# Kernel optimization log

Measured on AMD Instinct MI355X. Metric: run time of the kernel, lower is better.

## Reference

```python
import jax, jax.numpy as jnp
import numpy as np

TEMPERATURE = 8.0  # sqrt(d_k), d_k = 64

def setup_inputs() -> dict:
    key = jax.random.key(0)
    kq, kk, kv, km = jax.random.split(key, 4)
    B, H, S, D = 4, 16, 1024, 64
    q = jax.random.normal(kq, (B, H, S, D), dtype=jnp.float32)
    k = jax.random.normal(kk, (B, H, S, D), dtype=jnp.float32)
    v = jax.random.normal(kv, (B, H, S, D), dtype=jnp.float32)
    mask = jax.random.randint(km, (B, 1, S, S), 0, 2, dtype=jnp.int32)
    return {"q": q, "k": k, "v": v, "mask": mask}

def reference(q, k, v, mask):
    # scores: [B,H,S,S]
    attn = jnp.einsum("bhqd,bhkd->bhqk", q, k) / TEMPERATURE
    attn = jnp.where(mask == 0, jnp.float32(-1e9), attn)
    attn = jax.nn.softmax(attn, axis=-1)
    output = jnp.einsum("bhqk,bhkd->bhqd", attn, v)
    return (output, attn)
```

## Files before the change

### kernel.cpp

```cpp
#include <hip/hip_runtime.h>
#include <hip/hip_bf16.h>

#define S_LEN 1024
#define DH 64
#define QB 64
#define KT 64
#define NKT 16
#define LDP 72

typedef __attribute__((ext_vector_type(8))) short bf16x8;
typedef __attribute__((ext_vector_type(4))) float f32x4;
typedef unsigned long long u64;

__device__ __forceinline__ unsigned short f2bf(float f) {
  unsigned u = __float_as_uint(f);
  u = u + 0x7FFFu + ((u >> 16) & 1u);
  return (unsigned short)(u >> 16);
}
__device__ __forceinline__ float bf2f(unsigned short s) {
  return __uint_as_float((unsigned)s << 16);
}
__device__ __forceinline__ unsigned pk2(float a, float b) {
  __hip_bfloat162 h = __float22bfloat162_rn(float2{a, b});
  return *reinterpret_cast<unsigned*>(&h);
}

__global__ __launch_bounds__(256)
void maskpack_kernel(const int* __restrict__ mask, u64* __restrict__ bits) {
  int w    = blockIdx.x * 4 + (threadIdx.x >> 6);
  int lane = threadIdx.x & 63;
  int m = mask[(size_t)w * 64 + lane];
  u64 word = __ballot(m != 0);
  if (lane == 0) bits[w] = word;
}

__global__ __launch_bounds__(256, 4)
void sdpa_kernel(const float* __restrict__ qg, const float* __restrict__ kg,
                 const float* __restrict__ vg, const u64* __restrict__ bitsg,
                 float* __restrict__ outg, float* __restrict__ attng)
{
  __shared__ unsigned short Qs[QB][LDP];
  __shared__ unsigned short Ks[KT][LDP];
  __shared__ unsigned short Vt[DH][LDP];
  __shared__ unsigned short Ps[4][16][LDP];
  __shared__ float invLds[QB];

  const int tid  = threadIdx.x;
  const int wid  = tid >> 6;
  const int lane = tid & 63;
  const int lrow = lane & 15;
  const int lhi  = lane >> 4;

  const int blk = blockIdx.x;
  const int qbi = blk & 15;
  const int bh  = blk >> 4;
  const int b   = bh >> 4;

  const size_t qkv_off = (size_t)bh * (S_LEN * DH);
  const float* qb_ptr = qg + qkv_off + (size_t)qbi * QB * DH;
  const float* kb_ptr = kg + qkv_off;
  const float* vb_ptr = vg + qkv_off;
  const int q0 = qbi * QB;
  const int qrow_l = wid * 16 + lhi * 4;

  const u64* bptr = bitsg + ((size_t)(b * S_LEN + q0 + qrow_l)) * NKT;
  float* attn_base = attng + (size_t)bh * (S_LEN * S_LEN);

  float4 Kp[4];
  u64 Bc[4], Bn[4];
  #pragma unroll
  for (int i = 0; i < 4; ++i) {
    int idx = tid + 256 * i;
    Kp[i] = *(const float4*)(kb_ptr + (size_t)(idx >> 4) * DH + ((idx & 15) << 2));
  }
  #pragma unroll
  for (int r = 0; r < 4; ++r) Bc[r] = bptr[r * NKT + 0];

  #pragma unroll
  for (int i = 0; i < 4; ++i) {
    int idx = tid + 256 * i;
    int row = idx >> 4, c4 = (idx & 15) << 2;
    float4 t = *(const float4*)(qb_ptr + row * DH + c4);
    uint2 w; w.x = pk2(t.x, t.y); w.y = pk2(t.z, t.w);
    *(uint2*)&Qs[row][c4] = w;
  }
  __syncthreads();
  const bf16x8 qf0 = *(const bf16x8*)&Qs[wid * 16 + lrow][lhi * 8];
  const bf16x8 qf1 = *(const bf16x8*)&Qs[wid * 16 + lrow][32 + lhi * 8];

  float rs[4] = {0.f, 0.f, 0.f, 0.f};

  for (int kt = 0; kt < NKT; ++kt) {
    __syncthreads();
    #pragma unroll
    for (int i = 0; i < 4; ++i) {
      int idx = tid + 256 * i;
      int row = idx >> 4, c4 = (idx & 15) << 2;
      float4 t = Kp[i];
      uint2 w; w.x = pk2(t.x, t.y); w.y = pk2(t.z, t.w);
      *(uint2*)&Ks[row][c4] = w;
    }
    if (kt + 1 < NKT) {
      const float* kn = kb_ptr + (size_t)(kt + 1) * KT * DH;
      #pragma unroll
      for (int i = 0; i < 4; ++i) {
        int idx = tid + 256 * i;
        Kp[i] = *(const float4*)(kn + (size_t)(idx >> 4) * DH + ((idx & 15) << 2));
      }
      #pragma unroll
      for (int r = 0; r < 4; ++r) Bn[r] = bptr[r * NKT + kt + 1];
    }
    __syncthreads();

    #pragma unroll
    for (int nt = 0; nt < 4; ++nt) {
      bf16x8 kf0 = *(const bf16x8*)&Ks[nt * 16 + lrow][lhi * 8];
      bf16x8 kf1 = *(const bf16x8*)&Ks[nt * 16 + lrow][32 + lhi * 8];
      f32x4 acc = {0.f, 0.f, 0.f, 0.f};
      acc = __builtin_amdgcn_mfma_f32_16x16x32_bf16(qf0, kf0, acc, 0, 0, 0);
      acc = __builtin_amdgcn_mfma_f32_16x16x32_bf16(qf1, kf1, acc, 0, 0, 0);
      #pragma unroll
      for (int r = 0; r < 4; ++r) {
        bool ok = ((Bc[r] >> (nt * 16 + lrow)) & 1ull) != 0;
        float p = ok ? __expf(acc[r] * 0.125f) : 0.f;
        rs[r] += p;
      }
    }
    if (kt + 1 < NKT) {
      #pragma unroll
      for (int r = 0; r < 4; ++r) Bc[r] = Bn[r];
    }
  }

  #pragma unroll
  for (int r = 0; r < 4; ++r) {
    float v = rs[r];
    v += __shfl_xor(v, 1);
    v += __shfl_xor(v, 2);
    v += __shfl_xor(v, 4);
    v += __shfl_xor(v, 8);
    rs[r] = v;
  }
  float inv[4];
  #pragma unroll
  for (int r = 0; r < 4; ++r) inv[r] = 1.0f / rs[r];
  if (lrow == 0) {
    #pragma unroll
    for (int r = 0; r < 4; ++r) invLds[qrow_l + r] = inv[r];
  }

  float4 Vp[4];
  #pragma unroll
  for (int i = 0; i < 4; ++i) {
    int idx = tid + 256 * i;
    Kp[i] = *(const float4*)(kb_ptr + (size_t)(idx >> 4) * DH + ((idx & 15) << 2));
    Vp[i] = *(const float4*)(vb_ptr + (size_t)(idx & 63) * DH + ((idx >> 6) << 2));
  }
  #pragma unroll
  for (int r = 0; r < 4; ++r) Bc[r] = bptr[r * NKT + 0];

  f32x4 oacc[4];
  #pragma unroll
  for (int dt = 0; dt < 4; ++dt) oacc[dt] = (f32x4){0.f, 0.f, 0.f, 0.f};

  for (int kt = 0; kt < NKT; ++kt) {
    __syncthreads();

    #pragma unroll
    for (int i = 0; i < 4; ++i) {
      int idx = tid + 256 * i;
      int row = idx >> 4, c4 = (idx & 15) << 2;
      float4 t = Kp[i];
      uint2 w; w.x = pk2(t.x, t.y); w.y = pk2(t.z, t.w);
      *(uint2*)&Ks[row][c4] = w;
    }
    #pragma unroll
    for (int i = 0; i < 4; ++i) {
      int idx = tid + 256 * i;
      int row = idx & 63, c4 = (idx >> 6) << 2;
      float4 t = Vp[i];
      Vt[c4 + 0][row] = f2bf(t.x);
      Vt[c4 + 1][row] = f2bf(t.y);
      Vt[c4 + 2][row] = f2bf(t.z);
      Vt[c4 + 3][row] = f2bf(t.w);
    }
    if (kt + 1 < NKT) {
      const float* kn = kb_ptr + (size_t)(kt + 1) * KT * DH;
      const float* vn = vb_ptr + (size_t)(kt + 1) * KT * DH;
      #pragma unroll
      for (int i = 0; i < 4; ++i) {
        int idx = tid + 256 * i;
        Kp[i] = *(const float4*)(kn + (size_t)(idx >> 4) * DH + ((idx & 15) << 2));
        Vp[i] = *(const float4*)(vn + (size_t)(idx & 63) * DH + ((idx >> 6) << 2));
      }
      #pragma unroll
      for (int r = 0; r < 4; ++r) Bn[r] = bptr[r * NKT + kt + 1];
    }
    __syncthreads();

    #pragma unroll
    for (int nt = 0; nt < 4; ++nt) {
      bf16x8 kf0 = *(const bf16x8*)&Ks[nt * 16 + lrow][lhi * 8];
      bf16x8 kf1 = *(const bf16x8*)&Ks[nt * 16 + lrow][32 + lhi * 8];
      f32x4 acc = {0.f, 0.f, 0.f, 0.f};
      acc = __builtin_amdgcn_mfma_f32_16x16x32_bf16(qf0, kf0, acc, 0, 0, 0);
      acc = __builtin_amdgcn_mfma_f32_16x16x32_bf16(qf1, kf1, acc, 0, 0, 0);
      #pragma unroll
      for (int r = 0; r < 4; ++r) {
        bool ok = ((Bc[r] >> (nt * 16 + lrow)) & 1ull) != 0;
        float p = ok ? __expf(acc[r] * 0.125f) : 0.f;
        Ps[wid][lhi * 4 + r][nt * 16 + lrow] = f2bf(p);
      }
    }

    asm volatile("" ::: "memory");

    bf16x8 pf0 = *(const bf16x8*)&Ps[wid][lrow][lhi * 8];
    bf16x8 pf1 = *(const bf16x8*)&Ps[wid][lrow][32 + lhi * 8];
    #pragma unroll
    for (int dt = 0; dt < 4; ++dt) {
      bf16x8 vf0 = *(const bf16x8*)&Vt[dt * 16 + lrow][lhi * 8];
      bf16x8 vf1 = *(const bf16x8*)&Vt[dt * 16 + lrow][32 + lhi * 8];
      oacc[dt] = __builtin_amdgcn_mfma_f32_16x16x32_bf16(pf0, vf0, oacc[dt], 0, 0, 0);
      oacc[dt] = __builtin_amdgcn_mfma_f32_16x16x32_bf16(pf1, vf1, oacc[dt], 0, 0, 0);
    }

    {
      float* ab = attn_base + (size_t)(q0 + wid * 16) * S_LEN + kt * KT;
      #pragma unroll
      for (int j = 0; j < 4; ++j) {
        int flat = lane + 64 * j;
        int rowl = flat >> 4;
        int c4   = (flat & 15) << 2;
        float iv = invLds[wid * 16 + rowl];
        const unsigned short* pr = &Ps[wid][rowl][c4];
        f32x4 st;
        st[0] = bf2f(pr[0]) * iv;
        st[1] = bf2f(pr[1]) * iv;
        st[2] = bf2f(pr[2]) * iv;
        st[3] = bf2f(pr[3]) * iv;
        __builtin_nontemporal_store(st, (f32x4*)(ab + (size_t)rowl * S_LEN + c4));
      }
    }

    if (kt + 1 < NKT) {
      #pragma unroll
      for (int r = 0; r < 4; ++r) Bc[r] = Bn[r];
    }
  }

  #pragma unroll
  for (int dt = 0; dt < 4; ++dt)
    #pragma unroll
    for (int r = 0; r < 4; ++r)
      __builtin_nontemporal_store(oacc[dt][r] * inv[r],
          outg + qkv_off + (size_t)(q0 + qrow_l + r) * DH + dt * 16 + lrow);
}

extern "C" void kernel_launch(void* const* d_in, const int* in_sizes, int n_in,
                              void* d_out, int out_size, void* d_ws, size_t ws_size,
                              hipStream_t stream) {
  const float* q    = (const float*)d_in[0];
  const float* k    = (const float*)d_in[1];
  const float* v    = (const float*)d_in[2];
  const int*   mask = (const int*)d_in[3];
  float* out  = (float*)d_out;
  float* attn = out + (size_t)4 * 16 * 1024 * 64;

  const size_t nwords = (size_t)4 * S_LEN * NKT;
  u64* bits = (u64*)d_ws;
  maskpack_kernel<<<dim3(nwords / 4), dim3(256), 0, stream>>>(mask, bits);
  sdpa_kernel<<<dim3(64 * 16), dim3(256), 0, stream>>>(q, k, v, bits, out, attn);
}
```

Baseline: 128.5 us.

## Transpose QK MFMA so each lane stores its attention row directly from registers

Swaps the MFMA operand order so each lane holds four consecutive key columns of a single query row. The kernel can then write normalized attention probabilities straight from registers as float4 nontemporal stores, instead of round-tripping bf16 values through LDS and re-expanding them. The stored attention now keeps full fp32 precision. Each lane needs only one mask word, and the row-sum reduction shrinks to two shuffles. The P tile is still written to LDS as packed bf16 for the PV MFMA, and the output normalization reads the inverse sums back from LDS.

```diff
diff --git a/kernel.cpp b/kernel.cpp
--- a/kernel.cpp
+++ b/kernel.cpp
@@ -16,9 +16,6 @@
   unsigned u = __float_as_uint(f);
   u = u + 0x7FFFu + ((u >> 16) & 1u);
   return (unsigned short)(u >> 16);
-}
-__device__ __forceinline__ float bf2f(unsigned short s) {
-  return __uint_as_float((unsigned)s << 16);
 }
 __device__ __forceinline__ unsigned pk2(float a, float b) {
   __hip_bfloat162 h = __float22bfloat162_rn(float2{a, b});
@@ -62,19 +59,19 @@
   const float* vb_ptr = vg + qkv_off;
   const int q0 = qbi * QB;
   const int qrow_l = wid * 16 + lhi * 4;
-
-  const u64* bptr = bitsg + ((size_t)(b * S_LEN + q0 + qrow_l)) * NKT;
+  const int qrow_s = wid * 16 + lrow;
+
+  const u64* bptr = bitsg + (size_t)(b * S_LEN + qrow_s + q0) * NKT;
   float* attn_base = attng + (size_t)bh * (S_LEN * S_LEN);
 
   float4 Kp[4];
-  u64 Bc[4], Bn[4];
+  u64 Bw, Bn;
   #pragma unroll
   for (int i = 0; i < 4; ++i) {
     int idx = tid + 256 * i;
     Kp[i] = *(const float4*)(kb_ptr + (size_t)(idx >> 4) * DH + ((idx & 15) << 2));
   }
-  #pragma unroll
-  for (int r = 0; r < 4; ++r) Bc[r] = bptr[r * NKT + 0];
+  Bw = bptr[0];
 
   #pragma unroll
   for (int i = 0; i < 4; ++i) {
@@ -88,7 +85,7 @@
   const bf16x8 qf0 = *(const bf16x8*)&Qs[wid * 16 + lrow][lhi * 8];
   const bf16x8 qf1 = *(const bf16x8*)&Qs[wid * 16 + lrow][32 + lhi * 8];
 
-  float rs[4] = {0.f, 0.f, 0.f, 0.f};
+  float rs1 = 0.f;
 
   for (int kt = 0; kt < NKT; ++kt) {
     __syncthreads();
@@ -107,8 +104,7 @@
         int idx = tid + 256 * i;
         Kp[i] = *(const float4*)(kn + (size_t)(idx >> 4) * DH + ((idx & 15) << 2));
       }
-      #pragma unroll
-      for (int r = 0; r < 4; ++r) Bn[r] = bptr[r * NKT + kt + 1];
+      Bn = bptr[kt + 1];
     }
     __syncthreads();
 
@@ -117,37 +113,22 @@
       bf16x8 kf0 = *(const bf16x8*)&Ks[nt * 16 + lrow][lhi * 8];
       bf16x8 kf1 = *(const bf16x8*)&Ks[nt * 16 + lrow][32 + lhi * 8];
       f32x4 acc = {0.f, 0.f, 0.f, 0.f};
-      acc = __builtin_amdgcn_mfma_f32_16x16x32_bf16(qf0, kf0, acc, 0, 0, 0);
-      acc = __builtin_amdgcn_mfma_f32_16x16x32_bf16(qf1, kf1, acc, 0, 0, 0);
+      acc = __builtin_amdgcn_mfma_f32_16x16x32_bf16(kf0, qf0, acc, 0, 0, 0);
+      acc = __builtin_amdgcn_mfma_f32_16x16x32_bf16(kf1, qf1, acc, 0, 0, 0);
       #pragma unroll
       for (int r = 0; r < 4; ++r) {
-        bool ok = ((Bc[r] >> (nt * 16 + lrow)) & 1ull) != 0;
-        float p = ok ? __expf(acc[r] * 0.125f) : 0.f;
-        rs[r] += p;
-      }
-    }
-    if (kt + 1 < NKT) {
-      #pragma unroll
-      for (int r = 0; r < 4; ++r) Bc[r] = Bn[r];
-    }
-  }
-
-  #pragma unroll
-  for (int r = 0; r < 4; ++r) {
-    float v = rs[r];
-    v += __shfl_xor(v, 1);
-    v += __shfl_xor(v, 2);
-    v += __shfl_xor(v, 4);
-    v += __shfl_xor(v, 8);
-    rs[r] = v;
-  }
-  float inv[4];
-  #pragma unroll
-  for (int r = 0; r < 4; ++r) inv[r] = 1.0f / rs[r];
-  if (lrow == 0) {
-    #pragma unroll
-    for (int r = 0; r < 4; ++r) invLds[qrow_l + r] = inv[r];
-  }
+        int bit = nt * 16 + lhi * 4 + r;
+        float p = ((Bw >> bit) & 1ull) ? __expf(acc[r] * 0.125f) : 0.f;
+        rs1 += p;
+      }
+    }
+    if (kt + 1 < NKT) Bw = Bn;
+  }
+
+  rs1 += __shfl_xor(rs1, 16);
+  rs1 += __shfl_xor(rs1, 32);
+  const float invSelf = 1.0f / rs1;
+  if (lhi == 0) invLds[wid * 16 + lrow] = invSelf;
 
   float4 Vp[4];
   #pragma unroll
@@ -156,12 +137,13 @@
     Kp[i] = *(const float4*)(kb_ptr + (size_t)(idx >> 4) * DH + ((idx & 15) << 2));
     Vp[i] = *(const float4*)(vb_ptr + (size_t)(idx & 63) * DH + ((idx >> 6) << 2));
   }
-  #pragma unroll
-  for (int r = 0; r < 4; ++r) Bc[r] = bptr[r * NKT + 0];
+  Bw = bptr[0];
 
   f32x4 oacc[4];
   #pragma unroll
   for (int dt = 0; dt < 4; ++dt) oacc[dt] = (f32x4){0.f, 0.f, 0.f, 0.f};
+
+  float* alane = attn_base + (size_t)(q0 + qrow_s) * S_LEN + lhi * 4;
 
   for (int kt = 0; kt < NKT; ++kt) {
     __syncthreads();
@@ -193,8 +175,7 @@
         Kp[i] = *(const float4*)(kn + (size_t)(idx >> 4) * DH + ((idx & 15) << 2));
         Vp[i] = *(const float4*)(vn + (size_t)(idx & 63) * DH + ((idx >> 6) << 2));
       }
-      #pragma unroll
-      for (int r = 0; r < 4; ++r) Bn[r] = bptr[r * NKT + kt + 1];
+      Bn = bptr[kt + 1];
     }
     __syncthreads();
 
@@ -203,14 +184,20 @@
       bf16x8 kf0 = *(const bf16x8*)&Ks[nt * 16 + lrow][lhi * 8];
       bf16x8 kf1 = *(const bf16x8*)&Ks[nt * 16 + lrow][32 + lhi * 8];
       f32x4 acc = {0.f, 0.f, 0.f, 0.f};
-      acc = __builtin_amdgcn_mfma_f32_16x16x32_bf16(qf0, kf0, acc, 0, 0, 0);
-      acc = __builtin_amdgcn_mfma_f32_16x16x32_bf16(qf1, kf1, acc, 0, 0, 0);
+      acc = __builtin_amdgcn_mfma_f32_16x16x32_bf16(kf0, qf0, acc, 0, 0, 0);
+      acc = __builtin_amdgcn_mfma_f32_16x16x32_bf16(kf1, qf1, acc, 0, 0, 0);
+      float p[4];
       #pragma unroll
       for (int r = 0; r < 4; ++r) {
-        bool ok = ((Bc[r] >> (nt * 16 + lrow)) & 1ull) != 0;
-        float p = ok ? __expf(acc[r] * 0.125f) : 0.f;
-        Ps[wid][lhi * 4 + r][nt * 16 + lrow] = f2bf(p);
-      }
+        int bit = nt * 16 + lhi * 4 + r;
+        p[r] = ((Bw >> bit) & 1ull) ? __expf(acc[r] * 0.125f) : 0.f;
+      }
+      f32x4 st;
+      st[0] = p[0] * invSelf; st[1] = p[1] * invSelf;
+      st[2] = p[2] * invSelf; st[3] = p[3] * invSelf;
+      __builtin_nontemporal_store(st, (f32x4*)(alane + kt * KT + nt * 16));
+      uint2 w; w.x = pk2(p[0], p[1]); w.y = pk2(p[2], p[3]);
+      *(uint2*)&Ps[wid][lrow][nt * 16 + lhi * 4] = w;
     }
 
     asm volatile("" ::: "memory");
@@ -225,35 +212,17 @@
       oacc[dt] = __builtin_amdgcn_mfma_f32_16x16x32_bf16(pf1, vf1, oacc[dt], 0, 0, 0);
     }
 
-    {
-      float* ab = attn_base + (size_t)(q0 + wid * 16) * S_LEN + kt * KT;
-      #pragma unroll
-      for (int j = 0; j < 4; ++j) {
-        int flat = lane + 64 * j;
-        int rowl = flat >> 4;
-        int c4   = (flat & 15) << 2;
-        float iv = invLds[wid * 16 + rowl];
-        const unsigned short* pr = &Ps[wid][rowl][c4];
-        f32x4 st;
-        st[0] = bf2f(pr[0]) * iv;
-        st[1] = bf2f(pr[1]) * iv;
-        st[2] = bf2f(pr[2]) * iv;
-        st[3] = bf2f(pr[3]) * iv;
-        __builtin_nontemporal_store(st, (f32x4*)(ab + (size_t)rowl * S_LEN + c4));
-      }
-    }
-
-    if (kt + 1 < NKT) {
-      #pragma unroll
-      for (int r = 0; r < 4; ++r) Bc[r] = Bn[r];
-    }
-  }
-
+    if (kt + 1 < NKT) Bw = Bn;
+  }
+
+  float invOut[4];
+  #pragma unroll
+  for (int r = 0; r < 4; ++r) invOut[r] = invLds[qrow_l + r];
   #pragma unroll
   for (int dt = 0; dt < 4; ++dt)
     #pragma unroll
     for (int r = 0; r < 4; ++r)
-      __builtin_nontemporal_store(oacc[dt][r] * inv[r],
+      __builtin_nontemporal_store(oacc[dt][r] * invOut[r],
           outg + qkv_off + (size_t)(q0 + qrow_l + r) * DH + dt * 16 + lrow);
 }
 
```

Measured after the change: 165.4 us. +28.7%, slower.
